# Performance work log

Hardware: AMD Instinct MI355X
Metric: run time of the kernel (lower is better)

The kernel has to match this reference:

```python
import jax, jax.numpy as jnp
import numpy as np

B, S, D = 2, 2048, 1024
H = 16
HD = D // H
SCALE = HD ** (-0.5)


def setup_inputs() -> dict:
    key = jax.random.key(0)
    k1, k2, k3, k4 = jax.random.split(key, 4)
    x = jax.random.normal(k1, (B, S, D), dtype=jnp.float32)
    # nn.Linear-style init scale to keep activations sane
    w_qkv = jax.random.normal(k2, (3 * D, D), dtype=jnp.float32) * (D ** -0.5)
    w_out = jax.random.normal(k3, (D, D), dtype=jnp.float32) * (D ** -0.5)
    b_out = jax.random.normal(k4, (D,), dtype=jnp.float32) * 0.01
    return {"x": x, "w_qkv": w_qkv, "w_out": w_out, "b_out": b_out}


def reference(x, w_qkv, w_out, b_out):
    b, s, d = x.shape
    # qkv projection (no bias): [b, s, 3d]
    qkv = jnp.einsum('bsd,ed->bse', x, w_qkv)
    # Rearrange 'b c (e h hd) -> e b h c hd'
    qkv = qkv.reshape(b, s, 3, H, HD).transpose(2, 0, 3, 1, 4)
    # NOTE: original splits as (v, q, k) in that order
    v, q, k = qkv[0], qkv[1], qkv[2]
    # scale applied after matmul, as in the original
    scores = jnp.einsum('bhqd,bhkd->bhqk', q, k) * SCALE
    attn = jax.nn.softmax(scores, axis=-1)
    o = jnp.einsum('bhqk,bhkd->bhqd', attn, v)
    # 'b h c hd -> b c (h hd)'
    o = o.transpose(0, 2, 1, 3).reshape(b, s, d)
    return jnp.einsum('bsd,ed->bse', o, w_out) + b_out
```

## Files before the change

kernel.cpp:

```cpp
#include <hip/hip_runtime.h>
#include <cstdint>
#include <cstddef>

#define BB 2
#define SS 2048
#define DD 1024
#define HH 16
#define HDIM 64

typedef short bf16x8 __attribute__((ext_vector_type(8)));
typedef short bf16x4 __attribute__((ext_vector_type(4)));
typedef float f32x4 __attribute__((ext_vector_type(4)));
typedef float f32x2 __attribute__((ext_vector_type(2)));

union U4S8 { uint4 u; bf16x8 s; };
union U2S4 { uint2 u; bf16x4 s; unsigned short h[4]; };

#if defined(__HIP_DEVICE_COMPILE__)
# if __has_builtin(__builtin_amdgcn_exp2f)
#  define EXP2(x) __builtin_amdgcn_exp2f(x)
# else
#  define EXP2(x) exp2f(x)
# endif
#else
# define EXP2(x) exp2f(x)
#endif

__device__ __forceinline__ unsigned short f2bf(float f) {
    union { float f; unsigned int u; } c; c.f = f;
    unsigned int u = c.u;
    unsigned int r = (u + 0x7FFFu + ((u >> 16) & 1u)) >> 16;
    return (unsigned short)r;
}

__device__ __forceinline__ void async_cp16(const void* g, void* l) {
    __builtin_amdgcn_global_load_lds(
        (const __attribute__((address_space(1))) void*)g,
        (__attribute__((address_space(3))) void*)l, 16, 0, 0);
}

__global__ __launch_bounds__(256) void cvt_all(
    const float* __restrict__ x, const float* __restrict__ wq,
    const float* __restrict__ wo,
    unsigned short* __restrict__ xb, unsigned short* __restrict__ wqb,
    unsigned short* __restrict__ wob) {
    int i = blockIdx.x * 256 + threadIdx.x;
    const float* in; unsigned short* out; int j;
    if (i < 524288)       { in = x;  out = xb;  j = i; }
    else if (i < 917504)  { in = wq; out = wqb; j = i - 524288; }
    else                  { in = wo; out = wob; j = i - 917504; }
    float4 a = ((const float4*)in)[2 * j];
    float4 b = ((const float4*)in)[2 * j + 1];
    union { uint4 u; unsigned short h[8]; } o;
    o.h[0] = f2bf(a.x); o.h[1] = f2bf(a.y); o.h[2] = f2bf(a.z); o.h[3] = f2bf(a.w);
    o.h[4] = f2bf(b.x); o.h[5] = f2bf(b.y); o.h[6] = f2bf(b.z); o.h[7] = f2bf(b.w);
    ((uint4*)out)[j] = o.u;
}

__global__ __launch_bounds__(512, 2) void gemm_qkv(
    const unsigned short* __restrict__ A,
    const unsigned short* __restrict__ Bw,
    unsigned short* __restrict__ qb, unsigned short* __restrict__ kb,
    unsigned short* __restrict__ vb) {
    const int K = 1024;
    __shared__ unsigned short smem[65536];
    int tid = threadIdx.x;
    int lane = tid & 63, wave = tid >> 6;
    int wmp = wave & 1, wnp = wave >> 1;
    int lm = lane & 15, lq = lane >> 4;

    int id = blockIdx.y * 12 + blockIdx.x;
    int swz = (id & 7) * 24 + (id >> 3);
    int m0 = (swz / 12) * 256, n0 = (swz % 12) * 256;

    f32x4 acc[8][4] = {};

    int u2 = tid >> 2;
    int c2 = (tid & 3) ^ (u2 & 3);
    int sdst = tid * 8;
    const unsigned short* gA0 = A  + (size_t)(m0 + u2) * K + c2 * 8;
    const unsigned short* gB0 = Bw + (size_t)(n0 + u2) * K + c2 * 8;
    const unsigned short* gA1 = gA0 + (size_t)128 * K;
    const unsigned short* gB1 = gB0 + (size_t)128 * K;

#define STAGE4(j, kk) do {                                                  \
        async_cp16(gA0 + (kk), smem + (j) * 16384 + 0     + sdst);          \
        async_cp16(gA1 + (kk), smem + (j) * 16384 + 4096  + sdst);          \
        async_cp16(gB0 + (kk), smem + (j) * 16384 + 8192  + sdst);          \
        async_cp16(gB1 + (kk), smem + (j) * 16384 + 12288 + sdst);          \
    } while (0)

    int axk = (lq ^ (lm & 3)) * 8;
    int aBase = (wmp * 128 + lm) * 32 + axk;
    int bBase = 8192 + (wnp * 64 + lm) * 32 + axk;
    U4S8 af[8], bfr[4];

#define KT(j, kk3) do {                                                     \
        _Pragma("unroll")                                                   \
        for (int m = 0; m < 8; m++)                                         \
            af[m].u = *(const uint4*)(smem + (j) * 16384 + aBase + m * 512);\
        _Pragma("unroll")                                                   \
        for (int n = 0; n < 4; n++)                                         \
            bfr[n].u = *(const uint4*)(smem + (j) * 16384 + bBase + n * 512);\
        STAGE4((((j) + 3) & 3), kk3);                                       \
        _Pragma("unroll")                                                   \
        for (int m = 0; m < 8; m++)                                         \
            _Pragma("unroll")                                               \
            for (int n = 0; n < 4; n++)                                     \
                acc[m][n] = __builtin_amdgcn_mfma_f32_16x16x32_bf16(        \
                    af[m].s, bfr[n].s, acc[m][n], 0, 0, 0);                 \
        asm volatile("s_waitcnt vmcnt(8)" ::: "memory");                    \
        __builtin_amdgcn_s_barrier();                                       \
    } while (0)

    STAGE4(0, 0); STAGE4(1, 32); STAGE4(2, 64);
    asm volatile("s_waitcnt vmcnt(8)" ::: "memory");
    __builtin_amdgcn_s_barrier();

    #pragma unroll 1
    for (int t4 = 0; t4 < 8; ++t4) {
        int kb128 = t4 * 128;
        KT(0, kb128 + 96);
        KT(1, kb128 + 128);
        KT(2, kb128 + 160);
        KT(3, kb128 + 192);
    }
#undef KT
#undef STAGE4

    asm volatile("s_waitcnt vmcnt(0)" ::: "memory");
    __builtin_amdgcn_s_barrier();

    unsigned short* Lw = smem + wave * 8192;
    int wm = wmp * 128, wn = wnp * 64;
    int b = m0 >> 11;
    int s_base = (m0 + wm) & 2047;
    int h = ((n0 + wn) >> 6) & 15;
    if (n0 < 1024) {
        unsigned short* vdst = vb + ((size_t)(b * HH + h) * HDIM) * SS;
        #pragma unroll
        for (int c = 0; c < 2; c++) {
            #pragma unroll
            for (int m4 = 0; m4 < 4; m4++)
                #pragma unroll
                for (int ni = 0; ni < 4; ni++) {
                    U2S4 t;
                    #pragma unroll
                    for (int r = 0; r < 4; r++)
                        t.h[r] = f2bf(acc[c * 4 + m4][ni][r]);
                    *(uint2*)&Lw[(ni * 16 + lm) * 72 + m4 * 16 + lq * 4] = t.u;
                }
            __builtin_amdgcn_wave_barrier();
            #pragma unroll
            for (int it = 0; it < 8; it++) {
                int hd = it * 8 + (lane >> 3);
                int so = (lane & 7) * 8;
                uint4 val = *(const uint4*)&Lw[hd * 72 + so];
                *(uint4*)(vdst + (size_t)hd * SS + s_base + c * 64 + so) = val;
            }
            __builtin_amdgcn_wave_barrier();
        }
    } else {
        bool isq = n0 < 2048;
        unsigned short* dst = isq ? qb : kb;
        float scale = isq ? 0.18033688f : 1.0f;
        unsigned short* qdst = dst + ((size_t)(b * HH + h) * SS) * HDIM;
        #pragma unroll
        for (int c = 0; c < 2; c++) {
            #pragma unroll
            for (int m4 = 0; m4 < 4; m4++)
                #pragma unroll
                for (int ni = 0; ni < 4; ni++)
                    #pragma unroll
                    for (int r = 0; r < 4; r++)
                        Lw[(m4 * 16 + lq * 4 + r) * 72 + ni * 16 + lm] =
                            f2bf(acc[c * 4 + m4][ni][r] * scale);
            __builtin_amdgcn_wave_barrier();
            #pragma unroll
            for (int it = 0; it < 8; it++) {
                int srw = it * 8 + (lane >> 3);
                int so = (lane & 7) * 8;
                uint4 val = *(const uint4*)&Lw[srw * 72 + so];
                *(uint4*)(qdst + (size_t)(s_base + c * 64 + srw) * HDIM + so) = val;
            }
            __builtin_amdgcn_wave_barrier();
        }
    }
}

__global__ __launch_bounds__(512) void attn(
    const unsigned short* __restrict__ qb,
    const unsigned short* __restrict__ kb,
    const unsigned short* __restrict__ vb,
    unsigned short* __restrict__ ob) {
    int bh = blockIdx.y;
    int q0 = blockIdx.x * 128;
    int tid = threadIdx.x, lane = tid & 63, wave = tid >> 6;
    int grp = wave >> 2;
    int w4  = wave & 3;
    int lm = lane & 15, lq = lane >> 4;

    __shared__ unsigned short smem[32768];
    float* smf = (float*)smem;

    const unsigned short* qg = qb + (size_t)bh * SS * HDIM;
    const unsigned short* kg = kb + (size_t)bh * SS * HDIM;
    const unsigned short* vg = vb + (size_t)bh * HDIM * SS;

    U4S8 qf[2][2];
    #pragma unroll
    for (int qt = 0; qt < 2; qt++)
        #pragma unroll
        for (int ks = 0; ks < 2; ks++)
            qf[qt][ks].u = *(const uint4*)(
                qg + (size_t)(q0 + w4 * 32 + qt * 16 + lm) * HDIM + ks * 32 + lq * 8);

    f32x4 oacc[4][2] = {};
    f32x2 lsum2[2] = {};

    int lm7 = lm & 7;
    int kidx = lm * 64 + 8 * (lq ^ lm7);
    int vidx[2];
    #pragma unroll
    for (int kblk = 0; kblk < 2; kblk++)
        vidx[kblk] = lm * 64 + 8 * (((kblk << 2) | lq) ^ lm7);

    int sr  = tid >> 3;
    int s5  = sr & 31;
    int kap = (sr & 32) + (((s5 >> 2) & 3) << 3) + (((s5 >> 4) & 1) << 2) + (s5 & 3);
    int lch = (tid & 7) ^ (sr & 7);
    int sdst = tid * 8;
    const unsigned short* kpA = kg + (size_t)kap * HDIM + lch * 8;
    const unsigned short* kpB = kpA + 64 * HDIM;
    const unsigned short* vpA = vg + (size_t)sr * SS + lch * 8;
    const unsigned short* vpB = vpA + 64;

    #define STAGE(pbase)                                                       \
        do {                                                                   \
            async_cp16(kpA, smem + (pbase) + sdst);                            \
            async_cp16(kpB, smem + (pbase) + 4096 + sdst);                     \
            async_cp16(vpA, smem + (pbase) + 8192 + sdst);                     \
            async_cp16(vpB, smem + (pbase) + 12288 + sdst);                    \
            kpA += 128 * HDIM; kpB += 128 * HDIM; vpA += 128; vpB += 128;      \
        } while (0)

    STAGE(0);

    for (int kt = 0; kt < SS / 128; kt += 2) {
        #pragma unroll
        for (int hf = 0; hf < 2; hf++) {
            int cbase = hf ? 16384 : 0;
            int obase = hf ? 0 : 16384;
            __syncthreads();
            STAGE(obase);

            int kbase = cbase + grp * 4096;
            int vbase = cbase + 8192 + grp * 4096;

            U4S8 pb8[2][2];
            #pragma unroll
            for (int mi = 0; mi < 4; mi++) {
                U4S8 kf0, kf1;
                kf0.u = *(const uint4*)(smem + kbase + mi * 1024 + kidx);
                kf1.u = *(const uint4*)(smem + kbase + mi * 1024 + (kidx ^ 32));
                #pragma unroll
                for (int qt = 0; qt < 2; qt++) {
                    f32x4 sa = {};
                    sa = __builtin_amdgcn_mfma_f32_16x16x32_bf16(kf0.s, qf[qt][0].s, sa, 0, 0, 0);
                    sa = __builtin_amdgcn_mfma_f32_16x16x32_bf16(kf1.s, qf[qt][1].s, sa, 0, 0, 0);
                    float p0 = EXP2(sa[0]);
                    float p1 = EXP2(sa[1]);
                    float p2 = EXP2(sa[2]);
                    float p3 = EXP2(sa[3]);
                    f32x2 a01; a01[0] = p0; a01[1] = p1;
                    f32x2 a23; a23[0] = p2; a23[1] = p3;
                    lsum2[qt] += a01;
                    lsum2[qt] += a23;
                    unsigned int b0 = __float_as_uint(p0) + 0x8000u;
                    unsigned int b1 = __float_as_uint(p1) + 0x8000u;
                    unsigned int b2 = __float_as_uint(p2) + 0x8000u;
                    unsigned int b3 = __float_as_uint(p3) + 0x8000u;
                    unsigned int lo = __builtin_amdgcn_perm(b1, b0, 0x07060302u);
                    unsigned int hi = __builtin_amdgcn_perm(b3, b2, 0x07060302u);
                    if ((mi & 1) == 0) { pb8[mi >> 1][qt].u.x = lo; pb8[mi >> 1][qt].u.y = hi; }
                    else               { pb8[mi >> 1][qt].u.z = lo; pb8[mi >> 1][qt].u.w = hi; }
                }
            }

            #pragma unroll
            for (int mi2 = 0; mi2 < 4; mi2++) {
                #pragma unroll
                for (int kblk = 0; kblk < 2; kblk++) {
                    U4S8 vf;
                    vf.u = *(const uint4*)(smem + vbase + mi2 * 1024 + vidx[kblk]);
                    oacc[mi2][0] = __builtin_amdgcn_mfma_f32_16x16x32_bf16(
                        vf.s, pb8[kblk][0].s, oacc[mi2][0], 0, 0, 0);
                    oacc[mi2][1] = __builtin_amdgcn_mfma_f32_16x16x32_bf16(
                        vf.s, pb8[kblk][1].s, oacc[mi2][1], 0, 0, 0);
                }
            }
        }
    }
    #undef STAGE

    float gsum[2];
    #pragma unroll
    for (int qt = 0; qt < 2; qt++) {
        float s = lsum2[qt][0] + lsum2[qt][1];
        s += __shfl_xor(s, 16);
        s += __shfl_xor(s, 32);
        gsum[qt] = s;
    }

    __syncthreads();

    if (grp == 1) {
        float* pub = smf + w4 * 2048;
        #pragma unroll
        for (int mi2 = 0; mi2 < 4; mi2++)
            #pragma unroll
            for (int qt = 0; qt < 2; qt++)
                #pragma unroll
                for (int r = 0; r < 4; r++)
                    pub[(mi2 * 8 + qt * 4 + r) * 64 + lane] = oacc[mi2][qt][r];
        if (lq == 0) {
            smf[8192 + w4 * 32 + lm]      = gsum[0];
            smf[8192 + w4 * 32 + 16 + lm] = gsum[1];
        }
    }
    __syncthreads();

    if (grp == 0) {
        float* pub = smf + w4 * 2048;
        #pragma unroll
        for (int mi2 = 0; mi2 < 4; mi2++)
            #pragma unroll
            for (int qt = 0; qt < 2; qt++)
                #pragma unroll
                for (int r = 0; r < 4; r++)
                    oacc[mi2][qt][r] += pub[(mi2 * 8 + qt * 4 + r) * 64 + lane];
        float inv[2];
        inv[0] = 1.f / (gsum[0] + smf[8192 + w4 * 32 + lm]);
        inv[1] = 1.f / (gsum[1] + smf[8192 + w4 * 32 + 16 + lm]);

        unsigned short* Ow = smem + 17024 + w4 * 2304;
        #pragma unroll
        for (int mi2 = 0; mi2 < 4; mi2++)
            #pragma unroll
            for (int qt = 0; qt < 2; qt++) {
                U2S4 t;
                #pragma unroll
                for (int r = 0; r < 4; r++)
                    t.h[r] = f2bf(oacc[mi2][qt][r] * inv[qt]);
                *(uint2*)&Ow[(qt * 16 + lm) * 72 + mi2 * 16 + lq * 4] = t.u;
            }
        __builtin_amdgcn_wave_barrier();
        int b = bh >> 4, h = bh & 15;
        #pragma unroll
        for (int it = 0; it < 4; it++) {
            int q  = it * 8 + (lane >> 3);
            int off = (lane & 7) * 8;
            uint4 val = *(const uint4*)&Ow[q * 72 + off];
            int srw = q0 + w4 * 32 + q;
            *(uint4*)(ob + (size_t)(b * SS + srw) * DD + h * 64 + off) = val;
        }
    }
}

__global__ __launch_bounds__(256) void gemm_out(
    const unsigned short* __restrict__ A,
    const unsigned short* __restrict__ Bw,
    const float* __restrict__ bias, float* __restrict__ out) {
    const int K = 1024;
    __shared__ unsigned short smem[24576];
    int tid = threadIdx.x;
    int lane = tid & 63, wave = tid >> 6;
    int wm = (wave & 1) * 64, wn = (wave >> 1) * 32;
    int m0 = blockIdx.y * 128, n0 = blockIdx.x * 64;
    int lm = lane & 15, lq = lane >> 4;

    f32x4 acc[4][2] = {};

    int sdst = tid * 8;
    int lch = (tid & 3) ^ ((tid >> 3) & 3);
    const unsigned short* gA = A  + (size_t)(m0 + (tid >> 2)) * K + lch * 8;
    const unsigned short* gB = Bw + (size_t)(n0 + (tid >> 2)) * K + lch * 8;
    int sw = (lq ^ ((lm >> 1) & 3)) * 8;

#define OSTAGE(k0, buf) do {                                               \
        async_cp16(gA + (k0),               smem + (buf) + sdst);          \
        async_cp16(gA + 64 * K + (k0),      smem + (buf) + 2048 + sdst);   \
        async_cp16(gA + (k0) + 32,          smem + (buf) + 4096 + sdst);   \
        async_cp16(gA + 64 * K + (k0) + 32, smem + (buf) + 6144 + sdst);   \
        async_cp16(gB + (k0),               smem + (buf) + 8192 + sdst);   \
        async_cp16(gB + (k0) + 32,          smem + (buf) + 10240 + sdst);  \
    } while (0)

    OSTAGE(0, 0);
    for (int k0 = 0; k0 < K; k0 += 128) {
        #pragma unroll
        for (int hf = 0; hf < 2; hf++) {
            int base = hf ? 12288 : 0;
            int obuf = hf ? 0 : 12288;
            __syncthreads();
            int kn = k0 + 64 + hf * 64;
            if (kn < K) OSTAGE(kn, obuf);
            #pragma unroll
            for (int kc = 0; kc < 2; kc++) {
                const unsigned short* As = smem + base + kc * 4096;
                const unsigned short* Bs = smem + base + 8192 + kc * 2048;
                U4S8 af[4], bfx[2];
                #pragma unroll
                for (int i = 0; i < 4; i++)
                    af[i].u = *(const uint4*)(As + (wm + i * 16 + lm) * 32 + sw);
                #pragma unroll
                for (int i = 0; i < 2; i++)
                    bfx[i].u = *(const uint4*)(Bs + (wn + i * 16 + lm) * 32 + sw);
                #pragma unroll
                for (int mi = 0; mi < 4; mi++)
                    #pragma unroll
                    for (int ni = 0; ni < 2; ni++)
                        acc[mi][ni] = __builtin_amdgcn_mfma_f32_16x16x32_bf16(
                            af[mi].s, bfx[ni].s, acc[mi][ni], 0, 0, 0);
            }
        }
    }
#undef OSTAGE

    #pragma unroll
    for (int mi = 0; mi < 4; mi++) {
        int gr = m0 + wm + mi * 16 + lq * 4;
        #pragma unroll
        for (int ni = 0; ni < 2; ni++) {
            int gc = n0 + wn + ni * 16 + lm;
            float bv = bias[gc];
            #pragma unroll
            for (int r = 0; r < 4; r++)
                out[(size_t)(gr + r) * DD + gc] = acc[mi][ni][r] + bv;
        }
    }
}

extern "C" void kernel_launch(void* const* d_in, const int* in_sizes, int n_in,
                              void* d_out, int out_size, void* d_ws, size_t ws_size,
                              hipStream_t stream) {
    const float* x     = (const float*)d_in[0];
    const float* w_qkv = (const float*)d_in[1];
    const float* w_out = (const float*)d_in[2];
    const float* b_out = (const float*)d_in[3];
    float* out = (float*)d_out;

    unsigned short* ws = (unsigned short*)d_ws;
    const size_t NX = (size_t)BB * SS * DD;
    unsigned short* x_bf    = ws;
    unsigned short* wqkv_bf = x_bf + NX;
    unsigned short* wout_bf = wqkv_bf + 3145728;
    unsigned short* q_buf   = wout_bf + 1048576;
    unsigned short* k_buf   = q_buf + NX;
    unsigned short* v_buf   = k_buf + NX;
    unsigned short* o_buf   = v_buf + NX;

    cvt_all<<<4096, 256, 0, stream>>>(x, w_qkv, w_out, x_bf, wqkv_bf, wout_bf);
    gemm_qkv<<<dim3(12, 16), 512, 0, stream>>>(x_bf, wqkv_bf, q_buf, k_buf, v_buf);
    attn<<<dim3(16, 32), 512, 0, stream>>>(q_buf, k_buf, v_buf, o_buf);
    gemm_out<<<dim3(16, 32), 256, 0, stream>>>(o_buf, wout_bf, b_out, out);
}
```

Measured before the change: 178.6 us.

## Deepen K/V async prefetch to a four-stage ring buffer

Replaces the double-buffered K/V staging with a four-slot ring in a doubled shared-memory allocation. Three tiles are prefetched ahead, and partial vmcnt waits let in-flight copies overlap compute with a single barrier per tile. It also swaps the manual round-and-permute bf16 packing for the hardware v_cvt_pk_bf16_f32 instruction. The 128 KB of LDS per block lowers occupancy, and the loop now issues STAGE past the end of K/V (prefetching beyond tile 16), which risks out-of-bounds reads.

```diff
diff --git a/kernel.cpp b/kernel.cpp
--- a/kernel.cpp
+++ b/kernel.cpp
@@ -200,7 +200,7 @@
     int w4  = wave & 3;
     int lm = lane & 15, lq = lane >> 4;
 
-    __shared__ unsigned short smem[32768];
+    __shared__ unsigned short smem[65536];
     float* smf = (float*)smem;
 
     const unsigned short* qg = qb + (size_t)bh * SS * HDIM;
@@ -244,62 +244,60 @@
             kpA += 128 * HDIM; kpB += 128 * HDIM; vpA += 128; vpB += 128;      \
         } while (0)
 
-    STAGE(0);
-
-    for (int kt = 0; kt < SS / 128; kt += 2) {
-        #pragma unroll
-        for (int hf = 0; hf < 2; hf++) {
-            int cbase = hf ? 16384 : 0;
-            int obase = hf ? 0 : 16384;
-            __syncthreads();
-            STAGE(obase);
-
-            int kbase = cbase + grp * 4096;
-            int vbase = cbase + 8192 + grp * 4096;
-
-            U4S8 pb8[2][2];
-            #pragma unroll
-            for (int mi = 0; mi < 4; mi++) {
-                U4S8 kf0, kf1;
-                kf0.u = *(const uint4*)(smem + kbase + mi * 1024 + kidx);
-                kf1.u = *(const uint4*)(smem + kbase + mi * 1024 + (kidx ^ 32));
-                #pragma unroll
-                for (int qt = 0; qt < 2; qt++) {
-                    f32x4 sa = {};
-                    sa = __builtin_amdgcn_mfma_f32_16x16x32_bf16(kf0.s, qf[qt][0].s, sa, 0, 0, 0);
-                    sa = __builtin_amdgcn_mfma_f32_16x16x32_bf16(kf1.s, qf[qt][1].s, sa, 0, 0, 0);
-                    float p0 = EXP2(sa[0]);
-                    float p1 = EXP2(sa[1]);
-                    float p2 = EXP2(sa[2]);
-                    float p3 = EXP2(sa[3]);
-                    f32x2 a01; a01[0] = p0; a01[1] = p1;
-                    f32x2 a23; a23[0] = p2; a23[1] = p3;
-                    lsum2[qt] += a01;
-                    lsum2[qt] += a23;
-                    unsigned int b0 = __float_as_uint(p0) + 0x8000u;
-                    unsigned int b1 = __float_as_uint(p1) + 0x8000u;
-                    unsigned int b2 = __float_as_uint(p2) + 0x8000u;
-                    unsigned int b3 = __float_as_uint(p3) + 0x8000u;
-                    unsigned int lo = __builtin_amdgcn_perm(b1, b0, 0x07060302u);
-                    unsigned int hi = __builtin_amdgcn_perm(b3, b2, 0x07060302u);
-                    if ((mi & 1) == 0) { pb8[mi >> 1][qt].u.x = lo; pb8[mi >> 1][qt].u.y = hi; }
-                    else               { pb8[mi >> 1][qt].u.z = lo; pb8[mi >> 1][qt].u.w = hi; }
-                }
-            }
-
-            #pragma unroll
-            for (int mi2 = 0; mi2 < 4; mi2++) {
-                #pragma unroll
-                for (int kblk = 0; kblk < 2; kblk++) {
-                    U4S8 vf;
-                    vf.u = *(const uint4*)(smem + vbase + mi2 * 1024 + vidx[kblk]);
-                    oacc[mi2][0] = __builtin_amdgcn_mfma_f32_16x16x32_bf16(
-                        vf.s, pb8[kblk][0].s, oacc[mi2][0], 0, 0, 0);
-                    oacc[mi2][1] = __builtin_amdgcn_mfma_f32_16x16x32_bf16(
-                        vf.s, pb8[kblk][1].s, oacc[mi2][1], 0, 0, 0);
-                }
-            }
-        }
+    STAGE(0); STAGE(16384); STAGE(32768);
+    asm volatile("s_waitcnt vmcnt(8)" ::: "memory");
+    __builtin_amdgcn_s_barrier();
+
+    #pragma unroll 1
+    for (int t = 0; t < 16; ++t) {
+        int cb = (t & 3) << 14;
+        STAGE(((t + 3) & 3) << 14);
+
+        int kbase = cb + grp * 4096;
+        int vbase = cb + 8192 + grp * 4096;
+
+        U4S8 pb8[2][2];
+        #pragma unroll
+        for (int mi = 0; mi < 4; mi++) {
+            U4S8 kf0, kf1;
+            kf0.u = *(const uint4*)(smem + kbase + mi * 1024 + kidx);
+            kf1.u = *(const uint4*)(smem + kbase + mi * 1024 + (kidx ^ 32));
+            #pragma unroll
+            for (int qt = 0; qt < 2; qt++) {
+                f32x4 sa = {};
+                sa = __builtin_amdgcn_mfma_f32_16x16x32_bf16(kf0.s, qf[qt][0].s, sa, 0, 0, 0);
+                sa = __builtin_amdgcn_mfma_f32_16x16x32_bf16(kf1.s, qf[qt][1].s, sa, 0, 0, 0);
+                float p0 = EXP2(sa[0]);
+                float p1 = EXP2(sa[1]);
+                float p2 = EXP2(sa[2]);
+                float p3 = EXP2(sa[3]);
+                f32x2 a01; a01[0] = p0; a01[1] = p1;
+                f32x2 a23; a23[0] = p2; a23[1] = p3;
+                lsum2[qt] += a01;
+                lsum2[qt] += a23;
+                unsigned int lo, hi;
+                asm("v_cvt_pk_bf16_f32 %0, %1, %2" : "=v"(lo) : "v"(p0), "v"(p1));
+                asm("v_cvt_pk_bf16_f32 %0, %1, %2" : "=v"(hi) : "v"(p2), "v"(p3));
+                if ((mi & 1) == 0) { pb8[mi >> 1][qt].u.x = lo; pb8[mi >> 1][qt].u.y = hi; }
+                else               { pb8[mi >> 1][qt].u.z = lo; pb8[mi >> 1][qt].u.w = hi; }
+            }
+        }
+
+        #pragma unroll
+        for (int mi2 = 0; mi2 < 4; mi2++) {
+            #pragma unroll
+            for (int kblk = 0; kblk < 2; kblk++) {
+                U4S8 vf;
+                vf.u = *(const uint4*)(smem + vbase + mi2 * 1024 + vidx[kblk]);
+                oacc[mi2][0] = __builtin_amdgcn_mfma_f32_16x16x32_bf16(
+                    vf.s, pb8[kblk][0].s, oacc[mi2][0], 0, 0, 0);
+                oacc[mi2][1] = __builtin_amdgcn_mfma_f32_16x16x32_bf16(
+                    vf.s, pb8[kblk][1].s, oacc[mi2][1], 0, 0, 0);
+            }
+        }
+
+        asm volatile("s_waitcnt vmcnt(8)" ::: "memory");
+        __builtin_amdgcn_s_barrier();
     }
     #undef STAGE
 
@@ -312,6 +310,7 @@
         gsum[qt] = s;
     }
 
+    asm volatile("s_waitcnt vmcnt(0)" ::: "memory");
     __syncthreads();
 
     if (grp == 1) {
```

Measured after the change: 185.6 us. 3.9% more time.
